# Performance work log

Hardware: AMD Instinct MI355X
Metric: run time of the kernel (lower is better)

Reference implementation:

```python
import jax, jax.numpy as jnp
import numpy as np

B_SZ, D, HW, STRIDE, HEADS, DK, DV = 32, 64, 64, 4, 2, 32, 32
N = HW * HW                      # 4096 query tokens
M = (HW // STRIDE) ** 2          # 256 key/value tokens
EPS = 1e-5


def setup_inputs() -> dict:
    key = jax.random.key(0)
    ks = jax.random.split(key, 8)
    w = lambda k, s: jax.random.normal(k, s, dtype=jnp.float32) * 0.02
    return {
        "x": jax.random.normal(ks[0], (B_SZ, D, HW, HW), dtype=jnp.float32),
        "W_dw": jax.random.normal(ks[1], (D, 1, STRIDE, STRIDE), dtype=jnp.float32) * 0.1,
        "b_dw": jnp.zeros((D,), jnp.float32),
        "Wq": w(ks[2], (HEADS * DK, D)), "bq": jnp.zeros((HEADS * DK,), jnp.float32),
        "Wk": w(ks[3], (HEADS * DK, D)), "bk": jnp.zeros((HEADS * DK,), jnp.float32),
        "Wv": w(ks[4], (HEADS * DV, D)), "bv": jnp.zeros((HEADS * DV,), jnp.float32),
        "Wo": w(ks[5], (D, HEADS * DV)), "bo": jnp.zeros((D,), jnp.float32),
        "B": jax.random.normal(ks[6], (1, HEADS, N, M), dtype=jnp.float32),
    }


def reference(x, W_dw, b_dw, Wq, bq, Wk, bk, Wv, bv, Wo, bo, B):
    b, c, h, w = x.shape
    heads = B.shape[1]
    dk = Wq.shape[0] // heads
    dv = Wv.shape[0] // heads
    s = W_dw.shape[-1]

    # LayerNorm over (C, H, W), no affine params
    mu = jnp.mean(x, axis=(1, 2, 3), keepdims=True)
    var = jnp.mean((x - mu) ** 2, axis=(1, 2, 3), keepdims=True)
    xn = (x - mu) * jax.lax.rsqrt(var + EPS)

    # Q from normalized input: (b, N, c)
    xr = jnp.transpose(xn.reshape(b, c, h * w), (0, 2, 1))
    q = (xr @ Wq.T + bq).reshape(b, h * w, heads, dk).transpose(0, 2, 1, 3)

    # K/V from depthwise-conv downsample of the *unnormalized* x (as in source)
    kc = jax.lax.conv_general_dilated(
        x, W_dw, window_strides=(s, s), padding="VALID",
        feature_group_count=c,
        dimension_numbers=("NCHW", "OIHW", "NCHW"),
    ) + b_dw[None, :, None, None]
    kh, kw = kc.shape[2], kc.shape[3]
    kv_in = jnp.transpose(kc.reshape(b, c, kh * kw), (0, 2, 1))  # (b, M, c)
    k = (kv_in @ Wk.T + bk).reshape(b, kh * kw, heads, dk).transpose(0, 2, 1, 3)
    v = (kv_in @ Wv.T + bv).reshape(b, kh * kw, heads, dv).transpose(0, 2, 1, 3)

    # Attention with additive relative bias
    attn = jnp.einsum("bhid,bhjd->bhij", q, k) * (dk ** -0.5) + B
    attn = jax.nn.softmax(attn, axis=-1)
    tmp = jnp.einsum("bhij,bhjd->bhid", attn, v)           # (b, heads, N, dv)
    tmp = tmp.transpose(0, 2, 1, 3).reshape(b, h * w, heads * dv)

    # Output proj; NOTE: source does a raw .view(b, d, h, w) (reshape, not permute)
    out = (tmp @ Wo.T + bo).reshape(b, c, h, w)
    return out + x
```

## Files before the change

kernel.cpp:

```cpp
#include <hip/hip_runtime.h>

typedef float f32x4 __attribute__((ext_vector_type(4)));

#define MFMA8(a, b, c) __builtin_amdgcn_mfma_f32_16x16x32_fp8_fp8((long)(a), (long)(b), (c), 0, 0, 0)

__device__ __forceinline__ unsigned char f2fp8(float v) {
    int pk = __builtin_amdgcn_cvt_pk_fp8_f32(v, v, 0, false);
    return (unsigned char)(pk & 0xff);
}
__device__ __forceinline__ long packrow8(const float* p) {
    f32x4 a = *(const f32x4*)(p);
    f32x4 b = *(const f32x4*)(p + 4);
    int lo = __builtin_amdgcn_cvt_pk_fp8_f32(a.x, a.y, 0, false);
    lo = __builtin_amdgcn_cvt_pk_fp8_f32(a.z, a.w, lo, true);
    int hi = __builtin_amdgcn_cvt_pk_fp8_f32(b.x, b.y, 0, false);
    hi = __builtin_amdgcn_cvt_pk_fp8_f32(b.z, b.w, hi, true);
    return (long)(((unsigned long)(unsigned int)hi << 32) | (unsigned int)lo);
}
__device__ __forceinline__ int pack4(const float* p) {
    int v = __builtin_amdgcn_cvt_pk_fp8_f32(p[0], p[1], 0, false);
    return __builtin_amdgcn_cvt_pk_fp8_f32(p[2], p[3], v, true);
}

__global__ __launch_bounds__(512) void k_kvb2(
    const float* __restrict__ x, const float* __restrict__ Wdw, const float* __restrict__ bdw,
    const float* __restrict__ Wk, const float* __restrict__ bk,
    const float* __restrict__ Wv, const float* __restrict__ bv,
    unsigned char* __restrict__ Kg, unsigned char* __restrict__ Vg,
    float* __restrict__ part)
{
    __shared__ __align__(16) unsigned char Y[16 * 72];
    __shared__ float sm[16];
    const int mi = blockIdx.x, b = blockIdx.y;
    const int t = threadIdx.x, w = t >> 6, lane = t & 63;
    const int quad = lane >> 4, l = lane & 15;
    const float* xb = x + b * 262144;

    const int s2l = lane & 3, mjl = lane >> 2;
    float s = 0.f, ss = 0.f;
    #pragma unroll
    for (int ci = 0; ci < 8; ++ci) {
        int c = w * 8 + ci;
        float wd0 = Wdw[c * 16 + 0 + s2l];
        float wd1 = Wdw[c * 16 + 4 + s2l];
        float wd2 = Wdw[c * 16 + 8 + s2l];
        float wd3 = Wdw[c * 16 + 12 + s2l];
        const float* xr = xb + c * 4096 + mi * 256;
        float v0 = xr[lane], v1 = xr[64 + lane], v2 = xr[128 + lane], v3 = xr[192 + lane];
        s  += v0 + v1 + v2 + v3;
        ss += v0 * v0 + v1 * v1 + v2 * v2 + v3 * v3;
        float acc = v0 * wd0;
        acc = fmaf(v1, wd1, acc);
        acc = fmaf(v2, wd2, acc);
        acc = fmaf(v3, wd3, acc);
        acc += __shfl_xor(acc, 1);
        acc += __shfl_xor(acc, 2);
        if (s2l == 0) Y[mjl * 72 + c] = f2fp8(acc + bdw[c]);
    }
    #pragma unroll
    for (int off = 32; off > 0; off >>= 1) {
        s  += __shfl_down(s, off);
        ss += __shfl_down(ss, off);
    }
    if (lane == 0) { sm[w * 2] = s; sm[w * 2 + 1] = ss; }
    __syncthreads();
    if (t == 0) {
        float S = 0.f, SS = 0.f;
        #pragma unroll
        for (int i = 0; i < 8; ++i) { S += sm[i * 2]; SS += sm[i * 2 + 1]; }
        part[(b * 16 + mi) * 2]     = S;
        part[(b * 16 + mi) * 2 + 1] = SS;
    }

    long ya0 = *(const long*)(Y + l * 72 + quad * 8);
    long ya1 = *(const long*)(Y + l * 72 + 32 + quad * 8);
    if (w < 4) {
        int e4 = w;
        long f0 = packrow8(Wk + (e4 * 16 + l) * 64 + quad * 8);
        long f1 = packrow8(Wk + (e4 * 16 + l) * 64 + 32 + quad * 8);
        float bb = bk[e4 * 16 + l];
        f32x4 c = { bb, bb, bb, bb };
        c = MFMA8(ya0, f0, c);
        c = MFMA8(ya1, f1, c);
        unsigned char* kd = Kg + b * 16384 + (mi * 16 + quad * 4) * 64 + e4 * 16 + l;
        #pragma unroll
        for (int r = 0; r < 4; ++r) kd[r * 64] = f2fp8(c[r]);
    } else {
        int d4 = w - 4;
        long f0 = packrow8(Wv + (d4 * 16 + l) * 64 + quad * 8);
        long f1 = packrow8(Wv + (d4 * 16 + l) * 64 + 32 + quad * 8);
        f32x4 c = { bv[d4 * 16 + quad * 4 + 0], bv[d4 * 16 + quad * 4 + 1],
                    bv[d4 * 16 + quad * 4 + 2], bv[d4 * 16 + quad * 4 + 3] };
        c = MFMA8(f0, ya0, c);
        c = MFMA8(f1, ya1, c);
        unsigned char* vd = Vg + b * 16384 + (d4 * 16 + quad * 4) * 256 + mi * 16 + l;
        #pragma unroll
        for (int r = 0; r < 4; ++r) vd[r * 256] = f2fp8(c[r]);
    }
}

__global__ void k_prep0(const float* __restrict__ Wq, const float* __restrict__ Wo,
                        float* __restrict__ swq,
                        unsigned char* __restrict__ Wq8, unsigned char* __restrict__ Wo8)
{
    int t = threadIdx.x;
    {
        float f[16];
        #pragma unroll
        for (int g = 0; g < 4; ++g) *(f32x4*)&f[g * 4] = *(const f32x4*)(Wq + t * 16 + g * 4);
        uint4 o;
        o.x = pack4(&f[0]); o.y = pack4(&f[4]); o.z = pack4(&f[8]); o.w = pack4(&f[12]);
        *(uint4*)(Wq8 + t * 16) = o;
    }
    {
        float f[16];
        #pragma unroll
        for (int g = 0; g < 4; ++g) *(f32x4*)&f[g * 4] = *(const f32x4*)(Wo + t * 16 + g * 4);
        uint4 o;
        o.x = pack4(&f[0]); o.y = pack4(&f[4]); o.z = pack4(&f[8]); o.w = pack4(&f[12]);
        *(uint4*)(Wo8 + t * 16) = o;
    }
    if (t < 64) {
        float s = 0.f;
        for (int c = 0; c < 64; ++c) s += Wq[t * 64 + c];
        swq[t] = s;
    }
}

__global__ __launch_bounds__(512) void k_qgen(
    const float* __restrict__ x, const float* __restrict__ part,
    const float* __restrict__ bq, const float* __restrict__ swq,
    const unsigned char* __restrict__ Wq8, unsigned char* __restrict__ Qg)
{
    __shared__ __align__(16) unsigned char XS[256 * 72];
    const int seg = blockIdx.x, b = blockIdx.y;
    const int t = threadIdx.x, w = t >> 6, lane = t & 63;
    const int quad = lane >> 4, l = lane & 15;

    float S = 0.f, SS = 0.f;
    #pragma unroll
    for (int k = 0; k < 16; ++k) {
        S  += part[(b * 16 + k) * 2];
        SS += part[(b * 16 + k) * 2 + 1];
    }
    const float inv = 1.0f / 262144.0f;
    const float mu = S * inv;
    const float rstd = rsqrtf(SS * inv - mu * mu + 1e-5f);

    const int nb = seg * 256;
    const float* xb = x + b * 262144;
    #pragma unroll
    for (int ci = 0; ci < 8; ++ci) {
        int c = w * 8 + ci;
        const float* xr = xb + c * 4096 + nb;
        #pragma unroll
        for (int j = 0; j < 4; ++j)
            XS[(j * 64 + lane) * 72 + c] = f2fp8(xr[j * 64 + lane]);
    }
    long wqF[8];
    float qe[4];
    #pragma unroll
    for (int et = 0; et < 4; ++et) {
        wqF[et * 2 + 0] = *(const long*)(Wq8 + (et * 16 + l) * 64 + quad * 8);
        wqF[et * 2 + 1] = *(const long*)(Wq8 + (et * 16 + l) * 64 + 32 + quad * 8);
        qe[et] = bq[et * 16 + l] - rstd * mu * swq[et * 16 + l];
    }
    __syncthreads();

    unsigned char* Qb = Qg + b * 262144 + nb * 64;
    #pragma unroll
    for (int i = 0; i < 2; ++i) {
        int rt = w * 2 + i;
        long xa0 = *(const long*)(XS + (rt * 16 + l) * 72 + quad * 8);
        long xa1 = *(const long*)(XS + (rt * 16 + l) * 72 + 32 + quad * 8);
        #pragma unroll
        for (int et = 0; et < 4; ++et) {
            f32x4 c = { 0, 0, 0, 0 };
            c = MFMA8(xa0, wqF[et * 2 + 0], c);
            c = MFMA8(xa1, wqF[et * 2 + 1], c);
            unsigned char* qd = Qb + (rt * 16 + quad * 4) * 64 + et * 16 + l;
            #pragma unroll
            for (int r = 0; r < 4; ++r) qd[r * 64] = f2fp8(fmaf(rstd, c[r], qe[et]));
        }
    }
}

__global__ __launch_bounds__(512, 6) void k_attn4(
    const float* __restrict__ x, const unsigned char* __restrict__ Qg,
    const unsigned char* __restrict__ Wo8, const float* __restrict__ bo,
    const float* __restrict__ Bb, const unsigned char* __restrict__ Kg,
    const unsigned char* __restrict__ Vg, float* __restrict__ outp)
{
    __shared__ __align__(16) long smem8[5952];
    unsigned char* S = (unsigned char*)smem8;
    unsigned char* Kf = S;
    unsigned char* Vt = S + 20480;
    unsigned char* TS = S + 37888;
    const int tp = blockIdx.x, b = blockIdx.y;
    const int t = threadIdx.x, w = t >> 6, lane = t & 63;
    const int quad = lane >> 4, l = lane & 15;
    unsigned char* PS = S + 42496 + w * 640;
    const float* xb = x + b * 262144;
    const float SCALE = 0.17677669529663687f;

    const unsigned char* Kgb = Kg + b * 16384;
    const unsigned char* Vgb = Vg + b * 16384;
    #pragma unroll
    for (int r = 0; r < 2; ++r) {
        int idx = t + 512 * r;
        int m = idx >> 2, c16 = (idx & 3) * 16;
        *(uint4*)(Kf + m * 80 + c16) = *(const uint4*)(Kgb + m * 64 + c16);
        int d = idx >> 4, e16 = (idx & 15) * 16;
        *(uint4*)(Vt + d * 272 + e16) = *(const uint4*)(Vgb + d * 256 + e16);
    }
    const int rtq = w >> 1, ct0 = (w & 1) * 2;
    long woF[4];
    float bor[2];
    #pragma unroll
    for (int i = 0; i < 2; ++i) {
        woF[i * 2 + 0] = *(const long*)(Wo8 + ((ct0 + i) * 16 + l) * 64 + quad * 8);
        woF[i * 2 + 1] = *(const long*)(Wo8 + ((ct0 + i) * 16 + l) * 64 + 32 + quad * 8);
        bor[i] = bo[(ct0 + i) * 16 + l];
    }
    const int h = w & 1, nq = w >> 1;
    __syncthreads();

    for (int it = 0; it < 2; ++it) {
        const int tile = tp * 2 + it, n0 = tile * 64;
        long qa = *(const long*)(Qg + b * 262144 + (n0 + nq * 16 + l) * 64 + h * 32 + quad * 8);
        f32x4 O0 = { 0, 0, 0, 0 }, O1 = { 0, 0, 0, 0 };
        float Lp[4] = { 0, 0, 0, 0 };
        const float* Bbase = Bb + h * 1048576 + (n0 + nq * 16 + quad * 4) * 256;

        float Bv[2][4];
        #pragma unroll
        for (int sub = 0; sub < 2; ++sub)
            #pragma unroll
            for (int r = 0; r < 4; ++r)
                Bv[sub][r] = Bbase[r * 256 + sub * 16 + l];

        #pragma unroll 2
        for (int mc = 0; mc < 8; ++mc) {
            float Bn[2][4];
            if (mc < 7) {
                #pragma unroll
                for (int sub = 0; sub < 2; ++sub)
                    #pragma unroll
                    for (int r = 0; r < 4; ++r)
                        Bn[sub][r] = Bbase[r * 256 + (mc * 2 + 2 + sub) * 16 + l];
            }
            long kb0 = *(const long*)(Kf + ((mc * 2 + 0) * 16 + l) * 80 + h * 32 + quad * 8);
            long kb1 = *(const long*)(Kf + ((mc * 2 + 1) * 16 + l) * 80 + h * 32 + quad * 8);
            #pragma unroll
            for (int sub = 0; sub < 2; ++sub) {
                f32x4 sc = { 0, 0, 0, 0 };
                sc = MFMA8(qa, sub ? kb1 : kb0, sc);
                unsigned char* pw = PS + (quad * 4) * 40 + sub * 16 + l;
                #pragma unroll
                for (int r = 0; r < 4; ++r) {
                    float p = __expf(fmaf(sc[r], SCALE, Bv[sub][r]));
                    Lp[r] += p;
                    pw[r * 40] = f2fp8(p);
                }
            }
            long pa  = *(const long*)(PS + l * 40 + quad * 8);
            long vb0 = *(const long*)(Vt + (h * 32 + l) * 272 + mc * 32 + quad * 8);
            long vb1 = *(const long*)(Vt + (h * 32 + 16 + l) * 272 + mc * 32 + quad * 8);
            O0 = MFMA8(pa, vb0, O0);
            O1 = MFMA8(pa, vb1, O1);
            #pragma unroll
            for (int sub = 0; sub < 2; ++sub)
                #pragma unroll
                for (int r = 0; r < 4; ++r)
                    Bv[sub][r] = Bn[sub][r];
        }
        #pragma unroll
        for (int r = 0; r < 4; ++r) {
            #pragma unroll
            for (int d = 1; d < 16; d <<= 1) Lp[r] += __shfl_xor(Lp[r], d);
        }
        {
            unsigned char* td = TS + (nq * 16 + quad * 4) * 72 + h * 32 + l;
            #pragma unroll
            for (int r = 0; r < 4; ++r) {
                float inv = 1.0f / Lp[r];
                td[r * 72]      = f2fp8(O0[r] * inv);
                td[r * 72 + 16] = f2fp8(O1[r] * inv);
            }
        }
        __syncthreads();

        {
            long ta0 = *(const long*)(TS + (rtq * 16 + l) * 72 + quad * 8);
            long ta1 = *(const long*)(TS + (rtq * 16 + l) * 72 + 32 + quad * 8);
            float* ob = outp + b * 262144 + tile * 4096;
            const float* xr2 = xb + tile * 4096;
            #pragma unroll
            for (int i = 0; i < 2; ++i) {
                f32x4 c = { bor[i], bor[i], bor[i], bor[i] };
                c = MFMA8(ta0, woF[i * 2 + 0], c);
                c = MFMA8(ta1, woF[i * 2 + 1], c);
                #pragma unroll
                for (int r = 0; r < 4; ++r) {
                    int off = (rtq * 16 + quad * 4 + r) * 64 + (ct0 + i) * 16 + l;
                    ob[off] = c[r] + xr2[off];
                }
            }
        }
        __syncthreads();
    }
}

extern "C" void kernel_launch(void* const* d_in, const int* in_sizes, int n_in,
                              void* d_out, int out_size, void* d_ws, size_t ws_size,
                              hipStream_t stream) {
    (void)in_sizes; (void)n_in; (void)out_size; (void)ws_size;
    const float* x   = (const float*)d_in[0];
    const float* Wdw = (const float*)d_in[1];
    const float* bdw = (const float*)d_in[2];
    const float* Wq  = (const float*)d_in[3];
    const float* bq  = (const float*)d_in[4];
    const float* Wk  = (const float*)d_in[5];
    const float* bk  = (const float*)d_in[6];
    const float* Wv  = (const float*)d_in[7];
    const float* bv  = (const float*)d_in[8];
    const float* Wo  = (const float*)d_in[9];
    const float* bo  = (const float*)d_in[10];
    const float* Bb  = (const float*)d_in[11];
    float* outp = (float*)d_out;

    float* part = (float*)d_ws;
    float* swq  = (float*)((char*)d_ws + 4096);
    unsigned char* Wq8 = (unsigned char*)d_ws + 8192;
    unsigned char* Wo8 = (unsigned char*)d_ws + 12288;
    unsigned char* Kg  = (unsigned char*)d_ws + 16384;
    unsigned char* Vg  = Kg + 524288;
    unsigned char* Qg  = Vg + 524288;

    k_kvb2<<<dim3(16, 32), 512, 0, stream>>>(x, Wdw, bdw, Wk, bk, Wv, bv, Kg, Vg, part);
    k_prep0<<<1, 256, 0, stream>>>(Wq, Wo, swq, Wq8, Wo8);
    k_qgen<<<dim3(16, 32), 512, 0, stream>>>(x, part, bq, swq, Wq8, Qg);
    k_attn4<<<dim3(32, 32), 512, 0, stream>>>(x, Qg, Wo8, bo, Bb, Kg, Vg, outp);
}
```

Measured before the change: 155.5 us.

## Fuse Q projection into attention kernel and weight prep into KV kernel

Removes the separate weight-prep and Q-generation kernels. Weight fp8 packing now runs in one block of the KV kernel, and the attention kernel normalizes x and computes Q tiles in shared memory before the attention loop. This drops two launches and the global Q round-trip, at the cost of extra shared memory, two more barriers per tile, and re-reading x in the attention kernel. It also relies on implicit ordering between blocks of the first kernel for the packed weights, which the consuming kernel only reads after the launch boundary.

New measurement: 164.6 us. 5.8% more time.

```diff
diff --git a/kernel.cpp b/kernel.cpp
--- a/kernel.cpp
+++ b/kernel.cpp
@@ -22,12 +22,14 @@
     return __builtin_amdgcn_cvt_pk_fp8_f32(p[2], p[3], v, true);
 }
 
-__global__ __launch_bounds__(512) void k_kvb2(
+__global__ __launch_bounds__(512) void k_kvb3(
     const float* __restrict__ x, const float* __restrict__ Wdw, const float* __restrict__ bdw,
     const float* __restrict__ Wk, const float* __restrict__ bk,
     const float* __restrict__ Wv, const float* __restrict__ bv,
+    const float* __restrict__ Wq, const float* __restrict__ Wo,
     unsigned char* __restrict__ Kg, unsigned char* __restrict__ Vg,
-    float* __restrict__ part)
+    float* __restrict__ part, float* __restrict__ swq,
+    unsigned char* __restrict__ Wq8, unsigned char* __restrict__ Wo8)
 {
     __shared__ __align__(16) unsigned char Y[16 * 72];
     __shared__ float sm[16];
@@ -35,6 +37,26 @@
     const int t = threadIdx.x, w = t >> 6, lane = t & 63;
     const int quad = lane >> 4, l = lane & 15;
     const float* xb = x + b * 262144;
+
+    if (mi == 0 && b == 0) {
+        if (t < 256) {
+            float f[16];
+            #pragma unroll
+            for (int g = 0; g < 4; ++g) *(f32x4*)&f[g * 4] = *(const f32x4*)(Wq + t * 16 + g * 4);
+            uint4 o;
+            o.x = pack4(&f[0]); o.y = pack4(&f[4]); o.z = pack4(&f[8]); o.w = pack4(&f[12]);
+            *(uint4*)(Wq8 + t * 16) = o;
+            #pragma unroll
+            for (int g = 0; g < 4; ++g) *(f32x4*)&f[g * 4] = *(const f32x4*)(Wo + t * 16 + g * 4);
+            o.x = pack4(&f[0]); o.y = pack4(&f[4]); o.z = pack4(&f[8]); o.w = pack4(&f[12]);
+            *(uint4*)(Wo8 + t * 16) = o;
+        } else if (t < 320) {
+            int e = t - 256;
+            float s = 0.f;
+            for (int c = 0; c < 64; ++c) s += Wq[e * 64 + c];
+            swq[e] = s;
+        }
+    }
 
     const int s2l = lane & 3, mjl = lane >> 2;
     float s = 0.f, ss = 0.f;
@@ -99,109 +121,37 @@
     }
 }
 
-__global__ void k_prep0(const float* __restrict__ Wq, const float* __restrict__ Wo,
-                        float* __restrict__ swq,
-                        unsigned char* __restrict__ Wq8, unsigned char* __restrict__ Wo8)
-{
-    int t = threadIdx.x;
-    {
-        float f[16];
-        #pragma unroll
-        for (int g = 0; g < 4; ++g) *(f32x4*)&f[g * 4] = *(const f32x4*)(Wq + t * 16 + g * 4);
-        uint4 o;
-        o.x = pack4(&f[0]); o.y = pack4(&f[4]); o.z = pack4(&f[8]); o.w = pack4(&f[12]);
-        *(uint4*)(Wq8 + t * 16) = o;
-    }
-    {
-        float f[16];
-        #pragma unroll
-        for (int g = 0; g < 4; ++g) *(f32x4*)&f[g * 4] = *(const f32x4*)(Wo + t * 16 + g * 4);
-        uint4 o;
-        o.x = pack4(&f[0]); o.y = pack4(&f[4]); o.z = pack4(&f[8]); o.w = pack4(&f[12]);
-        *(uint4*)(Wo8 + t * 16) = o;
-    }
-    if (t < 64) {
-        float s = 0.f;
-        for (int c = 0; c < 64; ++c) s += Wq[t * 64 + c];
-        swq[t] = s;
-    }
-}
-
-__global__ __launch_bounds__(512) void k_qgen(
+__global__ __launch_bounds__(512, 6) void k_attn5(
     const float* __restrict__ x, const float* __restrict__ part,
     const float* __restrict__ bq, const float* __restrict__ swq,
-    const unsigned char* __restrict__ Wq8, unsigned char* __restrict__ Qg)
+    const unsigned char* __restrict__ Wq8, const unsigned char* __restrict__ Wo8,
+    const float* __restrict__ bo, const float* __restrict__ Bb,
+    const unsigned char* __restrict__ Kg, const unsigned char* __restrict__ Vg,
+    float* __restrict__ outp)
 {
-    __shared__ __align__(16) unsigned char XS[256 * 72];
-    const int seg = blockIdx.x, b = blockIdx.y;
-    const int t = threadIdx.x, w = t >> 6, lane = t & 63;
-    const int quad = lane >> 4, l = lane & 15;
-
-    float S = 0.f, SS = 0.f;
-    #pragma unroll
-    for (int k = 0; k < 16; ++k) {
-        S  += part[(b * 16 + k) * 2];
-        SS += part[(b * 16 + k) * 2 + 1];
-    }
-    const float inv = 1.0f / 262144.0f;
-    const float mu = S * inv;
-    const float rstd = rsqrtf(SS * inv - mu * mu + 1e-5f);
-
-    const int nb = seg * 256;
-    const float* xb = x + b * 262144;
-    #pragma unroll
-    for (int ci = 0; ci < 8; ++ci) {
-        int c = w * 8 + ci;
-        const float* xr = xb + c * 4096 + nb;
-        #pragma unroll
-        for (int j = 0; j < 4; ++j)
-            XS[(j * 64 + lane) * 72 + c] = f2fp8(xr[j * 64 + lane]);
-    }
-    long wqF[8];
-    float qe[4];
-    #pragma unroll
-    for (int et = 0; et < 4; ++et) {
-        wqF[et * 2 + 0] = *(const long*)(Wq8 + (et * 16 + l) * 64 + quad * 8);
-        wqF[et * 2 + 1] = *(const long*)(Wq8 + (et * 16 + l) * 64 + 32 + quad * 8);
-        qe[et] = bq[et * 16 + l] - rstd * mu * swq[et * 16 + l];
-    }
-    __syncthreads();
-
-    unsigned char* Qb = Qg + b * 262144 + nb * 64;
-    #pragma unroll
-    for (int i = 0; i < 2; ++i) {
-        int rt = w * 2 + i;
-        long xa0 = *(const long*)(XS + (rt * 16 + l) * 72 + quad * 8);
-        long xa1 = *(const long*)(XS + (rt * 16 + l) * 72 + 32 + quad * 8);
-        #pragma unroll
-        for (int et = 0; et < 4; ++et) {
-            f32x4 c = { 0, 0, 0, 0 };
-            c = MFMA8(xa0, wqF[et * 2 + 0], c);
-            c = MFMA8(xa1, wqF[et * 2 + 1], c);
-            unsigned char* qd = Qb + (rt * 16 + quad * 4) * 64 + et * 16 + l;
-            #pragma unroll
-            for (int r = 0; r < 4; ++r) qd[r * 64] = f2fp8(fmaf(rstd, c[r], qe[et]));
-        }
-    }
-}
-
-__global__ __launch_bounds__(512, 6) void k_attn4(
-    const float* __restrict__ x, const unsigned char* __restrict__ Qg,
-    const unsigned char* __restrict__ Wo8, const float* __restrict__ bo,
-    const float* __restrict__ Bb, const unsigned char* __restrict__ Kg,
-    const unsigned char* __restrict__ Vg, float* __restrict__ outp)
-{
-    __shared__ __align__(16) long smem8[5952];
+    __shared__ __align__(16) long smem8[6528];
     unsigned char* S = (unsigned char*)smem8;
     unsigned char* Kf = S;
     unsigned char* Vt = S + 20480;
+    unsigned char* XS = S + 37888;
+    unsigned char* QF = S + 42496;
     unsigned char* TS = S + 37888;
     const int tp = blockIdx.x, b = blockIdx.y;
     const int t = threadIdx.x, w = t >> 6, lane = t & 63;
     const int quad = lane >> 4, l = lane & 15;
-    unsigned char* PS = S + 42496 + w * 640;
+    unsigned char* PS = S + 47104 + w * 640;
     const float* xb = x + b * 262144;
     const float SCALE = 0.17677669529663687f;
+
+    float Ssum = 0.f, SSsum = 0.f;
+    #pragma unroll
+    for (int k = 0; k < 16; ++k) {
+        Ssum  += part[(b * 16 + k) * 2];
+        SSsum += part[(b * 16 + k) * 2 + 1];
+    }
+    const float invN = 1.0f / 262144.0f;
+    const float mu = Ssum * invN;
+    const float rstd = rsqrtf(SSsum * invN - mu * mu + 1e-5f);
 
     const unsigned char* Kgb = Kg + b * 16384;
     const unsigned char* Vgb = Vg + b * 16384;
@@ -214,20 +164,46 @@
         *(uint4*)(Vt + d * 272 + e16) = *(const uint4*)(Vgb + d * 256 + e16);
     }
     const int rtq = w >> 1, ct0 = (w & 1) * 2;
-    long woF[4];
-    float bor[2];
+    long wqF[4], woF[4];
+    float bqr[2], bor[2];
     #pragma unroll
     for (int i = 0; i < 2; ++i) {
+        wqF[i * 2 + 0] = *(const long*)(Wq8 + ((ct0 + i) * 16 + l) * 64 + quad * 8);
+        wqF[i * 2 + 1] = *(const long*)(Wq8 + ((ct0 + i) * 16 + l) * 64 + 32 + quad * 8);
         woF[i * 2 + 0] = *(const long*)(Wo8 + ((ct0 + i) * 16 + l) * 64 + quad * 8);
         woF[i * 2 + 1] = *(const long*)(Wo8 + ((ct0 + i) * 16 + l) * 64 + 32 + quad * 8);
+        bqr[i] = bq[(ct0 + i) * 16 + l];
         bor[i] = bo[(ct0 + i) * 16 + l];
     }
     const int h = w & 1, nq = w >> 1;
-    __syncthreads();
 
     for (int it = 0; it < 2; ++it) {
         const int tile = tp * 2 + it, n0 = tile * 64;
-        long qa = *(const long*)(Qg + b * 262144 + (n0 + nq * 16 + l) * 64 + h * 32 + quad * 8);
+
+        #pragma unroll
+        for (int ci = 0; ci < 8; ++ci) {
+            int c = w * 8 + ci;
+            float v = (xb[c * 4096 + n0 + lane] - mu) * rstd;
+            XS[lane * 72 + c] = f2fp8(v);
+        }
+        __syncthreads();
+
+        {
+            long xa0 = *(const long*)(XS + (rtq * 16 + l) * 72 + quad * 8);
+            long xa1 = *(const long*)(XS + (rtq * 16 + l) * 72 + 32 + quad * 8);
+            #pragma unroll
+            for (int i = 0; i < 2; ++i) {
+                f32x4 c = { bqr[i], bqr[i], bqr[i], bqr[i] };
+                c = MFMA8(xa0, wqF[i * 2 + 0], c);
+                c = MFMA8(xa1, wqF[i * 2 + 1], c);
+                unsigned char* qd = QF + (rtq * 16 + quad * 4) * 72 + (ct0 + i) * 16 + l;
+                #pragma unroll
+                for (int r = 0; r < 4; ++r) qd[r * 72] = f2fp8(c[r]);
+            }
+        }
+        __syncthreads();
+
+        long qa = *(const long*)(QF + (nq * 16 + l) * 72 + h * 32 + quad * 8);
         f32x4 O0 = { 0, 0, 0, 0 }, O1 = { 0, 0, 0, 0 };
         float Lp[4] = { 0, 0, 0, 0 };
         const float* Bbase = Bb + h * 1048576 + (n0 + nq * 16 + quad * 4) * 256;
@@ -335,10 +311,9 @@
     unsigned char* Wo8 = (unsigned char*)d_ws + 12288;
     unsigned char* Kg  = (unsigned char*)d_ws + 16384;
     unsigned char* Vg  = Kg + 524288;
-    unsigned char* Qg  = Vg + 524288;
-
-    k_kvb2<<<dim3(16, 32), 512, 0, stream>>>(x, Wdw, bdw, Wk, bk, Wv, bv, Kg, Vg, part);
-    k_prep0<<<1, 256, 0, stream>>>(Wq, Wo, swq, Wq8, Wo8);
-    k_qgen<<<dim3(16, 32), 512, 0, stream>>>(x, part, bq, swq, Wq8, Qg);
-    k_attn4<<<dim3(32, 32), 512, 0, stream>>>(x, Qg, Wo8, bo, Bb, Kg, Vg, outp);
-}
+
+    k_kvb3<<<dim3(16, 32), 512, 0, stream>>>(x, Wdw, bdw, Wk, bk, Wv, bv, Wq, Wo,
+                                             Kg, Vg, part, swq, Wq8, Wo8);
+    k_attn5<<<dim3(32, 32), 512, 0, stream>>>(x, part, bq, swq, Wq8, Wo8, bo, Bb,
+                                              Kg, Vg, outp);
+}
```
